# Kernel tuning notes

Hardware: AMD Instinct MI355X
Metric: run time of the kernel (lower is better)

Reference implementation:

```python
import jax, jax.numpy as jnp
import numpy as np

K = 16        # max_points
S = 3         # num_scales
D_MODEL = 256
KDIM = 16
TAU = 1e-4
B_BATCH = 512


def _boundaries(k):
    edges = [(i, j) for i in range(k) for j in range(i + 1, k)]
    tris = [(i, j, kk) for i in range(k) for j in range(i + 1, k) for kk in range(j + 1, k)]
    E, T = len(edges), len(tris)
    B1 = np.zeros((k, E), np.float32)
    for e, (i, j) in enumerate(edges):
        B1[i, e] = -1.0
        B1[j, e] = 1.0
    e2i = {e: idx for idx, e in enumerate(edges)}
    B2 = np.zeros((E, T), np.float32)
    for t, (i, j, kk) in enumerate(tris):
        B2[e2i[(j, kk)], t] = 1.0
        B2[e2i[(i, kk)], t] = -1.0
        B2[e2i[(i, j)], t] = 1.0
    e_i = np.array([e[0] for e in edges], np.int32)
    e_j = np.array([e[1] for e in edges], np.int32)
    t_ij = np.array([e2i[(a, b)] for (a, b, c) in tris], np.int32)
    t_jk = np.array([e2i[(b, c)] for (a, b, c) in tris], np.int32)
    t_ik = np.array([e2i[(a, c)] for (a, b, c) in tris], np.int32)
    return B1, B2, e_i, e_j, t_ij, t_jk, t_ik


def setup_inputs() -> dict:
    key = jax.random.key(0)
    ks = jax.random.split(key, 8)
    d = D_MODEL
    B1, B2, e_i, e_j, t_ij, t_jk, t_ik = _boundaries(K)

    def lin(kk, fin, fout):
        return jax.random.normal(kk, (fin, fout), jnp.float32) / np.sqrt(fin).astype(np.float32)

    return dict(
        x=jax.random.normal(ks[0], (B_BATCH, K, d), jnp.float32),
        mask=jnp.ones((B_BATCH, K), jnp.float32),
        B1=jnp.asarray(B1), B2=jnp.asarray(B2), abs_B1=jnp.asarray(np.abs(B1)),
        e_i=jnp.asarray(e_i), e_j=jnp.asarray(e_j),
        t_ij=jnp.asarray(t_ij), t_jk=jnp.asarray(t_jk), t_ik=jnp.asarray(t_ik),
        log_scales=jnp.linspace(-1.5, 1.5, S).astype(jnp.float32),
        Wg=lin(ks[1], d, KDIM), bg=jnp.zeros((KDIM,), jnp.float32),
        Wv0=lin(ks[2], d, d * S), bv0=jnp.zeros((d * S,), jnp.float32),
        We=lin(ks[3], d, d * S), be=jnp.zeros((d * S,), jnp.float32),
        Wout=lin(ks[4], 2 * S * d, d), bout=jnp.zeros((d,), jnp.float32),
        g1=jnp.ones((d,), jnp.float32), b1=jnp.zeros((d,), jnp.float32),
        g2=jnp.ones((d,), jnp.float32), b2=jnp.zeros((d,), jnp.float32),
        Wf1=lin(ks[5], d, 4 * d), bf1=jnp.zeros((4 * d,), jnp.float32),
        Wf2=lin(ks[6], 4 * d, d), bf2=jnp.zeros((d,), jnp.float32),
    )


def _layernorm(x, g, b):
    mu = jnp.mean(x, -1, keepdims=True)
    var = jnp.mean(jnp.square(x - mu), -1, keepdims=True)
    return (x - mu) * jax.lax.rsqrt(var + 1e-5) * g + b


def _forward(x, mask, B1, B2, abs_B1, e_i, e_j, t_ij, t_jk, t_ik,
             log_scales, Wg, bg, Wv0, bv0, We, be, Wout, bout,
             g1, b1, g2, b2, Wf1, bf1, Wf2, bf2):
    B, Kp, d = x.shape
    E = B1.shape[1]
    residual = x
    x_norm = _layernorm(x, g1, b1)
    P = x_norm @ Wg + bg                                   # (B,K,k_dim)
    mask2 = mask[:, :, None] * mask[:, None, :]            # (B,K,K)
    # cdist (safe sqrt: zero diag, no NaN grads)
    pn = jnp.sum(P * P, -1)
    d2 = jnp.maximum(pn[:, :, None] + pn[:, None, :] - 2.0 * jnp.einsum('bik,bjk->bij', P, P), 0.0)
    Dm = jnp.where(d2 > 0, jnp.sqrt(jnp.where(d2 > 0, d2, 1.0)), 0.0) * mask2
    sigma_sq = jnp.square(jnp.exp(log_scales))             # (S,)
    A = jnp.exp(-(Dm * Dm)[:, None] / (2.0 * sigma_sq[None, :, None, None] + 1e-8)) * mask2[:, None]  # (B,S,K,K)
    W1 = A[:, :, e_i, e_j]                                 # (B,S,E) edge gather
    W2 = W1[:, :, t_ij] * W1[:, :, t_jk] * W1[:, :, t_ik]  # (B,S,T) triangle weights
    V0 = (x_norm @ Wv0 + bv0).reshape(B, Kp, S, d).transpose(0, 2, 1, 3)         # (B,S,K,d)
    E_raw = jnp.einsum('ke,bkd->bed', abs_B1, x_norm)                            # (B,E,d)
    E_in = (E_raw @ We + be).reshape(B, E, S, d).transpose(0, 2, 1, 3)           # (B,S,E,d)
    # L0 = B1 diag(W1) B1^T + tau I
    L0 = jnp.einsum('ke,bse,me->bskm', B1, W1, B1) + TAU * jnp.eye(Kp, dtype=x.dtype)
    M0 = jnp.einsum('bskm,bsmd->bskd', L0, V0)
    # L1 = B1^T diag(mask) B1 + B2 diag(W2) B2^T + tau I
    term_down = jnp.einsum('ke,bk,kf->bef', B1, mask, B1)                        # (B,E,E)
    term_up = jnp.einsum('et,bst,ft->bsef', B2, W2, B2)                          # (B,S,E,E)
    L1 = term_down[:, None] + term_up + TAU * jnp.eye(E, dtype=x.dtype)
    M1 = jnp.einsum('bsef,bsfd->bsed', L1, E_in)
    M1n = jnp.einsum('ke,bsed->bskd', abs_B1, M1)                                # edges -> nodes
    node_cat = M0.transpose(0, 2, 1, 3).reshape(B, Kp, S * d)
    edge_cat = M1n.transpose(0, 2, 1, 3).reshape(B, Kp, S * d)
    attn = jnp.concatenate([node_cat, edge_cat], -1) @ Wout + bout
    x2 = residual + attn                                   # dropout is identity in eval
    h = jax.nn.gelu(_layernorm(x2, g2, b2) @ Wf1 + bf1, approximate=False) @ Wf2 + bf2
    return x2 + h


def reference(x, mask, B1, B2, abs_B1, e_i, e_j, t_ij, t_jk, t_ik,
              log_scales, Wg, bg, Wv0, bv0, We, be, Wout, bout,
              g1, b1, g2, b2, Wf1, bf1, Wf2, bf2):
    return _forward(x, mask, B1, B2, abs_B1, e_i, e_j, t_ij, t_jk, t_ik,
                    log_scales, Wg, bg, Wv0, bv0, We, be, Wout, bout,
                    g1, b1, g2, b2, Wf1, bf1, Wf2, bf2)
```

## Files before the change

### kernel.cpp

```cpp
#include <hip/hip_runtime.h>
#include <math.h>

#define KN 16
#define DM 256
#define NS 3
#define NE 120
#define NT_TRI 560
#define NBATCH 512
#define TAUF 1e-4f
#define KAUG 1600

typedef unsigned short ushort_t;
typedef __attribute__((ext_vector_type(8))) short short8v;
typedef __attribute__((ext_vector_type(4))) short short4v;
typedef __attribute__((ext_vector_type(4))) float f32x4;

#define OFF_WSTACK 0u
#define OFF_WF1T   819200u
#define OFF_WF2T   1343488u
#define OFF_TOPO   1867776u
#define OFF_Z      1875968u
#define OFF_H      1875968u
#define OFF_LN2    28090368u

__device__ __forceinline__ ushort_t f2bf(float f) {
    union { float f; unsigned int u; } v; v.f = f;
    unsigned int r = v.u + 0x7FFFu + ((v.u >> 16) & 1u);
    return (ushort_t)(r >> 16);
}
__device__ __forceinline__ void gload_lds16(const void* g, void* l) {
    auto gp = (const __attribute__((address_space(1))) unsigned int*)(unsigned long long)(g);
    auto lp = (__attribute__((address_space(3))) unsigned int*)(unsigned long long)(l);
    __builtin_amdgcn_global_load_lds(gp, lp, 16, 0, 0);
}

__global__ __launch_bounds__(256) void prep_kernel(
    const float* __restrict__ Wv0, const float* __restrict__ bv0,
    const float* __restrict__ We,  const float* __restrict__ be,
    const float* __restrict__ Wout,
    const float* __restrict__ Wf1, const float* __restrict__ Wf2,
    const int* __restrict__ e_i, const int* __restrict__ e_j,
    const int* __restrict__ t_ij, const int* __restrict__ t_jk, const int* __restrict__ t_ik,
    ushort_t* __restrict__ wstack, ushort_t* __restrict__ wf1t,
    ushort_t* __restrict__ wf2t,
    float* __restrict__ topoF, int* __restrict__ triPk)
{
    __shared__ float lhs[16][DM];
    __shared__ float tile[64][65];
    __shared__ int   eidxL[256];
    const int bid = blockIdx.x;
    const int j = threadIdx.x;

    if (bid == 230) {
        eidxL[j] = -1;
        __syncthreads();
        if (j < NE) {
            const int i = e_i[j], jn = e_j[j];
            eidxL[i*16 + jn] = j; eidxL[jn*16 + i] = j;
        }
        __syncthreads();
        const int n = j >> 4, m = j & 15;
        float q, p2, adj;
        if (n != m) {
            const int e = eidxL[j];
            if (e >= 0) { q = (m == e_j[e]) ? 1.f : -1.f; p2 = 1.f; adj = 1.f; }
            else        { q = 0.f; p2 = 0.f; adj = 0.f; }
        } else {
            q = 0.f; p2 = 0.f; adj = 0.f;
            for (int kk = 0; kk < KN; ++kk) {
                if (kk == n) continue;
                const int e = eidxL[n*16 + kk];
                if (e >= 0) { q += (n == e_j[e]) ? 1.f : -1.f; p2 += 1.f; }
            }
        }
        topoF[j] = q; topoF[256 + j] = p2; topoF[512 + j] = adj;
        for (int tt = j; tt < NT_TRI; tt += 256) {
            const int eij = t_ij[tt], ejk = t_jk[tt], eik = t_ik[tt];
            const int a0 = e_i[eij], a1 = e_j[eij];
            const int b0 = e_i[ejk], b1v = e_j[ejk];
            const int c0 = e_i[eik], c1 = e_j[eik];
            const int mid = (b0 == a0 || b0 == a1) ? b0 : b1v;
            triPk[2*tt]   = a0 | (a1 << 8) | (b0 << 16) | (b1v << 24);
            triPk[2*tt+1] = c0 | (c1 << 8) | (mid << 16);
        }
        return;
    }

    if (bid < 102) {
        const int m = bid / 17, by = bid % 17;
        const int path = m / 3, s = m % 3;
        const float* __restrict__ Wo = Wout + (size_t)m*DM*DM;
        if (by == 16) {
            const float* bv = (path == 0) ? bv0 : be;
            const float f = (path == 0) ? 1.0f : 0.5f;
            float acc = 0.f;
            for (int k = 0; k < DM; ++k)
                acc += bv[s*DM + k] * f * Wo[k*DM + j];
            wstack[(size_t)j*KAUG + 1536 + m] = f2bf(acc);
            if (m == 0)
                for (int c = 1542; c < KAUG; ++c)
                    wstack[(size_t)j*KAUG + c] = 0;
            return;
        }
        const float* src = (path == 0) ? Wv0 : We;
        const int i0 = by * 16;
        for (int r = 0; r < 16; ++r)
            lhs[r][j] = src[(size_t)(i0 + r)*(NS*DM) + s*DM + j];
        __syncthreads();
        float acc[16];
#pragma unroll
        for (int r = 0; r < 16; ++r) acc[r] = 0.f;
        for (int k = 0; k < DM; ++k) {
            const float w = Wo[k*DM + j];
#pragma unroll
            for (int r = 0; r < 16; ++r) acc[r] += lhs[r][k] * w;
        }
#pragma unroll
        for (int r = 0; r < 16; ++r)
            wstack[(size_t)j*KAUG + m*DM + i0 + r] = f2bf(acc[r]);
        return;
    }

    const float* in; ushort_t* outp; int R, C, rt, ct;
    if (bid < 166) {
        const int q = bid - 102;
        in = Wf1; outp = wf1t; R = 256; C = 1024;
        rt = (q >> 4) * 64; ct = (q & 15) * 64;
    } else {
        const int q = bid - 166;
        in = Wf2; outp = wf2t; R = 1024; C = 256;
        rt = (q >> 2) * 64; ct = (q & 3) * 64;
    }
#pragma unroll
    for (int q2 = 0; q2 < 16; ++q2) {
        const int idx = q2*256 + j;
        const int r = idx >> 6, c = idx & 63;
        tile[r][c] = in[(size_t)(rt + r)*C + ct + c];
    }
    __syncthreads();
#pragma unroll
    for (int q2 = 0; q2 < 16; ++q2) {
        const int idx = q2*256 + j;
        const int cc = idx >> 6, rr = idx & 63;
        outp[(size_t)(ct + cc)*R + rt + rr] = f2bf(tile[rr][cc]);
    }
}

__global__ __launch_bounds__(256) void attn_topo_kernel(
    const float* __restrict__ x, const float* __restrict__ mask,
    const float* __restrict__ log_scales,
    const float* __restrict__ Wg, const float* __restrict__ bg,
    const float* __restrict__ g1, const float* __restrict__ b1,
    const float* __restrict__ topoF, const int* __restrict__ triPk,
    ushort_t* __restrict__ Z)
{
    const int b = blockIdx.x;
    const int t = threadIdx.x;
    const int n = t >> 4, m = t & 15;

    __shared__ ushort_t xnbT[DM][16];
    __shared__ float Plds[KN][KN];
    __shared__ float mskL[KN];
    __shared__ float QL[256];
    __shared__ float P2L[256];
    __shared__ float adjL[256];
    __shared__ float sA[NS][KN][KN];
    __shared__ float Hupd[NS*KN];
    __shared__ ushort_t Tbf[6][KN][32];

    QL[t]  = topoF[t];
    P2L[t] = topoF[256 + t];
    adjL[t] = topoF[512 + t];
    if (t < KN) mskL[t] = mask[b*KN + t];

    float xv[16];
    {
        const int cg = m * 16;
        const float* xr = x + (size_t)(b*KN + n)*DM + cg;
        const f32x4 v0 = *(const f32x4*)(xr);
        const f32x4 v1 = *(const f32x4*)(xr + 4);
        const f32x4 v2 = *(const f32x4*)(xr + 8);
        const f32x4 v3 = *(const f32x4*)(xr + 12);
#pragma unroll
        for (int q = 0; q < 4; ++q) { xv[q] = v0[q]; xv[4+q] = v1[q]; xv[8+q] = v2[q]; xv[12+q] = v3[q]; }
        float ssum = 0.f;
#pragma unroll
        for (int q = 0; q < 16; ++q) ssum += xv[q];
#pragma unroll
        for (int o = 1; o < 16; o <<= 1) ssum += __shfl_xor(ssum, o);
        const float mu = ssum * (1.f/DM);
        float vsum = 0.f;
#pragma unroll
        for (int q = 0; q < 16; ++q) { const float d = xv[q]-mu; vsum += d*d; }
#pragma unroll
        for (int o = 1; o < 16; o <<= 1) vsum += __shfl_xor(vsum, o);
        const float rstd = rsqrtf(vsum*(1.f/DM) + 1e-5f);
        const f32x4 ga = *(const f32x4*)(g1 + cg),   gb = *(const f32x4*)(g1 + cg + 4);
        const f32x4 gc = *(const f32x4*)(g1 + cg + 8), gd = *(const f32x4*)(g1 + cg + 12);
        const f32x4 ba = *(const f32x4*)(b1 + cg),   bb = *(const f32x4*)(b1 + cg + 4);
        const f32x4 bc = *(const f32x4*)(b1 + cg + 8), bd = *(const f32x4*)(b1 + cg + 12);
        float gg[16], bbv[16];
#pragma unroll
        for (int q = 0; q < 4; ++q) {
            gg[q] = ga[q]; gg[4+q] = gb[q]; gg[8+q] = gc[q]; gg[12+q] = gd[q];
            bbv[q] = ba[q]; bbv[4+q] = bb[q]; bbv[8+q] = bc[q]; bbv[12+q] = bd[q];
        }
#pragma unroll
        for (int q = 0; q < 16; ++q) {
            xv[q] = (xv[q]-mu)*rstd*gg[q] + bbv[q];
            xnbT[cg + q][n] = f2bf(xv[q]);
        }
    }

    {
        float part[16];
#pragma unroll
        for (int c = 0; c < 16; ++c) part[c] = 0.f;
        const int cg = m * 16;
#pragma unroll
        for (int q = 0; q < 16; ++q) {
            const float xq = xv[q];
            const float* wr = Wg + (size_t)(cg + q)*KN;
            const f32x4 w0 = *(const f32x4*)(wr);
            const f32x4 w1 = *(const f32x4*)(wr + 4);
            const f32x4 w2 = *(const f32x4*)(wr + 8);
            const f32x4 w3 = *(const f32x4*)(wr + 12);
            part[0]  += xq*w0[0]; part[1]  += xq*w0[1]; part[2]  += xq*w0[2]; part[3]  += xq*w0[3];
            part[4]  += xq*w1[0]; part[5]  += xq*w1[1]; part[6]  += xq*w1[2]; part[7]  += xq*w1[3];
            part[8]  += xq*w2[0]; part[9]  += xq*w2[1]; part[10] += xq*w2[2]; part[11] += xq*w2[3];
            part[12] += xq*w3[0]; part[13] += xq*w3[1]; part[14] += xq*w3[2]; part[15] += xq*w3[3];
        }
        const int b0 = t & 1, b1b = (t>>1)&1, b2 = (t>>2)&1, b3 = (t>>3)&1;
        float p8[8];
#pragma unroll
        for (int c2 = 0; c2 < 8; ++c2) {
            const float keep = b0 ? part[2*c2+1] : part[2*c2];
            const float send = b0 ? part[2*c2]   : part[2*c2+1];
            p8[c2] = keep + __shfl_xor(send, 1);
        }
        float p4[4];
#pragma unroll
        for (int c2 = 0; c2 < 4; ++c2) {
            const float keep = b1b ? p8[2*c2+1] : p8[2*c2];
            const float send = b1b ? p8[2*c2]   : p8[2*c2+1];
            p4[c2] = keep + __shfl_xor(send, 2);
        }
        float p2v[2];
#pragma unroll
        for (int c2 = 0; c2 < 2; ++c2) {
            const float keep = b2 ? p4[2*c2+1] : p4[2*c2];
            const float send = b2 ? p4[2*c2]   : p4[2*c2+1];
            p2v[c2] = keep + __shfl_xor(send, 4);
        }
        const float keep = b3 ? p2v[1] : p2v[0];
        const float send = b3 ? p2v[0] : p2v[1];
        Plds[n][m] = keep + __shfl_xor(send, 8) + bg[m];
    }
    __syncthreads();

    float T0[NS], hq;
    {
        float d2 = 0.f;
#pragma unroll
        for (int k = 0; k < KN; ++k) {
            const float dd = Plds[n][k] - Plds[m][k];
            d2 += dd*dd;
        }
        const float m2v = mskL[n]*mskL[m];
        const float dm = (d2 > 0.f) ? sqrtf(d2)*m2v : 0.f;
        const float dmsq = dm*dm;
        const float adjv = adjL[t];
#pragma unroll
        for (int s = 0; s < NS; ++s) {
            const float sig2 = expf(2.f*log_scales[s]);
            const float a = expf(-dmsq/(2.f*sig2 + 1e-8f)) * m2v;
            sA[s][n][m] = a;
            const float am = a * adjv;
            float rsum = am;
#pragma unroll
            for (int o = 1; o < 16; o <<= 1) rsum += __shfl_xor(rsum, o);
            const float tv = (m == n) ? (TAUF + rsum) : (-am);
            T0[s] = tv;
            Tbf[s][n][m] = f2bf(tv);
        }
        hq = 0.f;
#pragma unroll
        for (int k = 0; k < KN; ++k)
            hq += mskL[k]*QL[n*16 + k]*QL[m*16 + k];
        if (t < NS*KN) Hupd[t] = 0.f;
#pragma unroll
        for (int idx = 0; idx < 6; ++idx) {
            const int e2 = idx*256 + t;
            Tbf[e2 >> 8][(e2 >> 4) & 15][16 + (e2 & 15)] = 0;
        }
    }
    __syncthreads();

    for (int tt = t; tt < NT_TRI; tt += 256) {
        const int w0 = triPk[2*tt], w1 = triPk[2*tt+1];
        const int a0 = w0 & 255, a1 = (w0 >> 8) & 255;
        const int b0 = (w0 >> 16) & 255, b1v = (w0 >> 24) & 255;
        const int c0 = w1 & 255, c1 = (w1 >> 8) & 255, mid = (w1 >> 16) & 255;
#pragma unroll
        for (int s = 0; s < NS; ++s)
            atomicAdd(&Hupd[s*KN + mid],
                      4.f * sA[s][a0][a1] * sA[s][b0][b1v] * sA[s][c0][c1]);
    }
    __syncthreads();

    ushort_t* Zb = Z + (size_t)b*KN*KAUG;
    {
        float T1[NS];
        const float p2v = P2L[t];
#pragma unroll
        for (int s = 0; s < NS; ++s) {
            const float tv = hq + TAUF*p2v + ((m == n) ? Hupd[s*KN + n] : 0.f);
            T1[s] = tv;
            Tbf[NS + s][n][m] = f2bf(tv);
        }
        float sv[6] = {T0[0], T0[1], T0[2], T1[0], T1[1], T1[2]};
#pragma unroll
        for (int q = 0; q < 6; ++q) {
            float v = sv[q];
#pragma unroll
            for (int o = 1; o < 16; o <<= 1) v += __shfl_xor(v, o);
            sv[q] = v;
        }
        const float wv = (m==0)?sv[0]:(m==1)?sv[1]:(m==2)?sv[2]:(m==3)?sv[3]:(m==4)?sv[4]:sv[5];
        if (m < 6) Zb[(size_t)n*KAUG + 1536 + m] = f2bf(wv);
        for (int idx = t; idx < 58*KN; idx += 256) {
            const int nn = idx / 58, c = 1542 + idx % 58;
            Zb[(size_t)nn*KAUG + c] = 0;
        }
    }
    __syncthreads();

    {
        const int w = t >> 6, l = t & 63;
        const int lr = l & 15, lk = l >> 4;
        short8v bfr[4];
#pragma unroll
        for (int q4 = 0; q4 < 4; ++q4) {
            const int jc = w*64 + q4*16 + lr;
            bfr[q4] = *(const short8v*)&xnbT[jc][(lk & 1)*8];
        }
#pragma unroll
        for (int m6 = 0; m6 < 6; ++m6) {
            const short8v af = *(const short8v*)&Tbf[m6][lr][lk*8];
#pragma unroll
            for (int q4 = 0; q4 < 4; ++q4) {
                f32x4 acc = {0.f,0.f,0.f,0.f};
                acc = __builtin_amdgcn_mfma_f32_16x16x32_bf16(af, bfr[q4], acc, 0, 0, 0);
                const int jc = w*64 + q4*16 + lr;
#pragma unroll
                for (int rg = 0; rg < 4; ++rg)
                    Zb[(size_t)(lk*4 + rg)*KAUG + m6*256 + jc] = f2bf(acc[rg]);
            }
        }
    }
}

template<int BM, int BN, int KD, int EPI>
__global__ __launch_bounds__(256) void gemm_lds(
    const ushort_t* __restrict__ A, const ushort_t* __restrict__ Bt,
    const float* __restrict__ bias, const float* __restrict__ resid,
    float* __restrict__ outF, ushort_t* __restrict__ outH, int ldo)
{
    constexpr int BK = 64;
    constexpr int MF = BM / 32, NF = BN / 32;
    __shared__ ushort_t lA[BM*BK];
    __shared__ ushort_t lB[BN*BK];
    const int t = threadIdx.x;
    const int w = t >> 6, l = t & 63;
    const int wm = w & 1, wn = w >> 1;
    const int lr = l & 15, lk = l >> 4;
    const int brow = blockIdx.x * BM;
    const int bcol = blockIdx.y * BN;

    f32x4 acc[MF][NF];
#pragma unroll
    for (int mf = 0; mf < MF; ++mf)
#pragma unroll
        for (int nt = 0; nt < NF; ++nt)
            acc[mf][nt] = (f32x4){0.f,0.f,0.f,0.f};

    const int byteoff = t * 16;

    for (int kc = 0; kc < KD/BK; ++kc) {
        if (kc) __syncthreads();
#pragma unroll
        for (int c = 0; c < BM/32; ++c) {
            const int bo = c*4096 + byteoff;
            const int row = bo >> 7, kb = bo & 127;
            gload_lds16(A + (size_t)(brow + row)*KD + kc*BK + (kb >> 1), lA + (bo >> 1));
        }
#pragma unroll
        for (int c = 0; c < BN/32; ++c) {
            const int bo = c*4096 + byteoff;
            const int row = bo >> 7, kb = bo & 127;
            gload_lds16(Bt + (size_t)(bcol + row)*KD + kc*BK + (kb >> 1), lB + (bo >> 1));
        }
        __syncthreads();
#pragma unroll
        for (int ks = 0; ks < 2; ++ks) {
            short8v af[MF], bfr[NF];
#pragma unroll
            for (int mf = 0; mf < MF; ++mf)
                af[mf] = *(const short8v*)(lA + (wm*(BM/2) + mf*16 + lr)*BK + ks*32 + lk*8);
#pragma unroll
            for (int nt = 0; nt < NF; ++nt)
                bfr[nt] = *(const short8v*)(lB + (wn*(BN/2) + nt*16 + lr)*BK + ks*32 + lk*8);
#pragma unroll
            for (int mf = 0; mf < MF; ++mf)
#pragma unroll
                for (int nt = 0; nt < NF; ++nt)
                    acc[mf][nt] = __builtin_amdgcn_mfma_f32_16x16x32_bf16(
                        af[mf], bfr[nt], acc[mf][nt], 0, 0, 0);
        }
    }

#pragma unroll
    for (int mf = 0; mf < MF; ++mf) {
#pragma unroll
        for (int nt = 0; nt < NF; ++nt) {
            const int col = bcol + wn*(BN/2) + nt*16 + lr;
#pragma unroll
            for (int rg = 0; rg < 4; ++rg) {
                const int row = brow + wm*(BM/2) + mf*16 + lk*4 + rg;
                const size_t o = (size_t)row * ldo + col;
                const float v = acc[mf][nt][rg];
                if (EPI == 1) {
                    const float u = v + bias[col];
                    const float a = 0.79788456080286536f*(u + 0.044715f*u*u*u);
                    outH[o] = f2bf(u / (1.f + __expf(-2.f*a)));
                } else if (EPI == 2) {
                    outF[o] = outF[o] + v + bias[col];
                } else {
                    outF[o] = resid[o] + v + bias[col];
                }
            }
        }
    }
}

__global__ __launch_bounds__(256) void ln_rows_kernel(
    const float* __restrict__ in, const float* __restrict__ g,
    const float* __restrict__ bvec, ushort_t* __restrict__ outv)
{
    const int row = blockIdx.x*4 + (threadIdx.x >> 6);
    const int l = threadIdx.x & 63;
    const float4 v = *(const float4*)(in + (size_t)row*DM + l*4);
    float s = v.x + v.y + v.z + v.w;
#pragma unroll
    for (int o = 1; o < 64; o <<= 1) s += __shfl_xor(s, o);
    const float mu = s * (1.f/DM);
    float d0 = v.x-mu, d1 = v.y-mu, d2 = v.z-mu, d3 = v.w-mu;
    float vs = d0*d0 + d1*d1 + d2*d2 + d3*d3;
#pragma unroll
    for (int o = 1; o < 64; o <<= 1) vs += __shfl_xor(vs, o);
    const float rstd = rsqrtf(vs*(1.f/DM) + 1e-5f);
    short4v o4;
    o4[0] = (short)f2bf(d0*rstd*g[l*4+0] + bvec[l*4+0]);
    o4[1] = (short)f2bf(d1*rstd*g[l*4+1] + bvec[l*4+1]);
    o4[2] = (short)f2bf(d2*rstd*g[l*4+2] + bvec[l*4+2]);
    o4[3] = (short)f2bf(d3*rstd*g[l*4+3] + bvec[l*4+3]);
    *(short4v*)(outv + (size_t)row*DM + l*4) = o4;
}

extern "C" void kernel_launch(void* const* d_in, const int* in_sizes, int n_in,
                              void* d_out, int out_size, void* d_ws, size_t ws_size,
                              hipStream_t stream) {
    const float* x          = (const float*)d_in[0];
    const float* mask       = (const float*)d_in[1];
    const int*   e_i        = (const int*)  d_in[5];
    const int*   e_j        = (const int*)  d_in[6];
    const int*   t_ij       = (const int*)  d_in[7];
    const int*   t_jk       = (const int*)  d_in[8];
    const int*   t_ik       = (const int*)  d_in[9];
    const float* log_scales = (const float*)d_in[10];
    const float* Wg         = (const float*)d_in[11];
    const float* bg         = (const float*)d_in[12];
    const float* Wv0        = (const float*)d_in[13];
    const float* bv0        = (const float*)d_in[14];
    const float* We         = (const float*)d_in[15];
    const float* be         = (const float*)d_in[16];
    const float* Wout       = (const float*)d_in[17];
    const float* bout       = (const float*)d_in[18];
    const float* g1         = (const float*)d_in[19];
    const float* b1         = (const float*)d_in[20];
    const float* g2         = (const float*)d_in[21];
    const float* b2         = (const float*)d_in[22];
    const float* Wf1        = (const float*)d_in[23];
    const float* bf1        = (const float*)d_in[24];
    const float* Wf2        = (const float*)d_in[25];
    const float* bf2        = (const float*)d_in[26];

    char* wsb = (char*)d_ws;
    ushort_t* wstack = (ushort_t*)(wsb + OFF_WSTACK);
    ushort_t* wf1t   = (ushort_t*)(wsb + OFF_WF1T);
    ushort_t* wf2t   = (ushort_t*)(wsb + OFF_WF2T);
    float*    topoF  = (float*)   (wsb + OFF_TOPO);
    int*      triPk  = (int*)     (wsb + OFF_TOPO + 3072);
    ushort_t* Z      = (ushort_t*)(wsb + OFF_Z);
    ushort_t* H      = (ushort_t*)(wsb + OFF_H);
    ushort_t* ln2    = (ushort_t*)(wsb + OFF_LN2);
    float*    out    = (float*)d_out;

    hipLaunchKernelGGL(prep_kernel, dim3(231), dim3(256), 0, stream,
                       Wv0, bv0, We, be, Wout, Wf1, Wf2,
                       e_i, e_j, t_ij, t_jk, t_ik,
                       wstack, wf1t, wf2t, topoF, triPk);
    hipLaunchKernelGGL(attn_topo_kernel, dim3(NBATCH), dim3(256), 0, stream,
                       x, mask, log_scales, Wg, bg, g1, b1, topoF, triPk, Z);
    hipLaunchKernelGGL((gemm_lds<64,64,KAUG,3>), dim3(128,4), dim3(256), 0, stream,
                       Z, wstack, bout, x, out, (ushort_t*)nullptr, 256);
    hipLaunchKernelGGL(ln_rows_kernel, dim3(2048), dim3(256), 0, stream,
                       out, g2, b2, ln2);
    hipLaunchKernelGGL((gemm_lds<128,128,256,1>), dim3(64,8), dim3(256), 0, stream,
                       ln2, wf1t, bf1, (const float*)nullptr,
                       (float*)nullptr, H, 1024);
    hipLaunchKernelGGL((gemm_lds<64,64,1024,2>), dim3(128,4), dim3(256), 0, stream,
                       H, wf2t, bf2, (const float*)nullptr,
                       out, (ushort_t*)nullptr, 256);
}
```

Before: 122.2 us.

## Fuse LayerNorm into FFN1 GEMM, swizzle LDS tiles, widen K-chunk, vectorize Z stores

The standalone LayerNorm kernel is folded into a new FFN1 GEMM that normalizes its 64-row A tile into LDS before the MMA loop. This removes one launch and the bf16 round trip of the normalized activations through global memory. The generic GEMM gains a BK template parameter, set to 128 for the two remaining instances, plus an XOR swizzle on LDS tiles to avoid bank conflicts. The attention kernel swaps its MFMA operands so Z is written as packed short4 vectors, padding the K dimension to 1664 (and xnbT to 32 columns) with zeros. The costs are more K-padding work in the first GEMM and more LDS per block, which may lower occupancy.

```diff
diff --git a/kernel.cpp b/kernel.cpp
--- a/kernel.cpp
+++ b/kernel.cpp
@@ -8,7 +8,7 @@
 #define NT_TRI 560
 #define NBATCH 512
 #define TAUF 1e-4f
-#define KAUG 1600
+#define KAUG 1664
 
 typedef unsigned short ushort_t;
 typedef __attribute__((ext_vector_type(8))) short short8v;
@@ -16,12 +16,11 @@
 typedef __attribute__((ext_vector_type(4))) float f32x4;
 
 #define OFF_WSTACK 0u
-#define OFF_WF1T   819200u
-#define OFF_WF2T   1343488u
-#define OFF_TOPO   1867776u
-#define OFF_Z      1875968u
-#define OFF_H      1875968u
-#define OFF_LN2    28090368u
+#define OFF_WF1T   851968u
+#define OFF_WF2T   1376256u
+#define OFF_TOPO   1900544u
+#define OFF_Z      1908736u
+#define OFF_H      1908736u
 
 __device__ __forceinline__ ushort_t f2bf(float f) {
     union { float f; unsigned int u; } v; v.f = f;
@@ -158,7 +157,7 @@
     const int t = threadIdx.x;
     const int n = t >> 4, m = t & 15;
 
-    __shared__ ushort_t xnbT[DM][16];
+    __shared__ ushort_t xnbT[DM][32];
     __shared__ float Plds[KN][KN];
     __shared__ float mskL[KN];
     __shared__ float QL[256];
@@ -172,6 +171,11 @@
     P2L[t] = topoF[256 + t];
     adjL[t] = topoF[512 + t];
     if (t < KN) mskL[t] = mask[b*KN + t];
+    {
+        const short8v z8 = {0,0,0,0,0,0,0,0};
+        *(short8v*)&xnbT[t][16] = z8;
+        *(short8v*)&xnbT[t][24] = z8;
+    }
 
     float xv[16];
     {
@@ -328,8 +332,8 @@
         }
         const float wv = (m==0)?sv[0]:(m==1)?sv[1]:(m==2)?sv[2]:(m==3)?sv[3]:(m==4)?sv[4]:sv[5];
         if (m < 6) Zb[(size_t)n*KAUG + 1536 + m] = f2bf(wv);
-        for (int idx = t; idx < 58*KN; idx += 256) {
-            const int nn = idx / 58, c = 1542 + idx % 58;
+        for (int idx = t; idx < 122*KN; idx += 256) {
+            const int nn = idx / 122, c = 1542 + idx % 122;
             Zb[(size_t)nn*KAUG + c] = 0;
         }
     }
@@ -338,36 +342,38 @@
     {
         const int w = t >> 6, l = t & 63;
         const int lr = l & 15, lk = l >> 4;
-        short8v bfr[4];
+        short8v bfrT[6];
+#pragma unroll
+        for (int m6 = 0; m6 < 6; ++m6)
+            bfrT[m6] = *(const short8v*)&Tbf[m6][lr][lk*8];
 #pragma unroll
         for (int q4 = 0; q4 < 4; ++q4) {
-            const int jc = w*64 + q4*16 + lr;
-            bfr[q4] = *(const short8v*)&xnbT[jc][(lk & 1)*8];
-        }
-#pragma unroll
-        for (int m6 = 0; m6 < 6; ++m6) {
-            const short8v af = *(const short8v*)&Tbf[m6][lr][lk*8];
-#pragma unroll
-            for (int q4 = 0; q4 < 4; ++q4) {
+            const int jb = w*64 + q4*16;
+            const short8v axn = *(const short8v*)&xnbT[jb + lr][lk*8];
+#pragma unroll
+            for (int m6 = 0; m6 < 6; ++m6) {
                 f32x4 acc = {0.f,0.f,0.f,0.f};
-                acc = __builtin_amdgcn_mfma_f32_16x16x32_bf16(af, bfr[q4], acc, 0, 0, 0);
-                const int jc = w*64 + q4*16 + lr;
-#pragma unroll
-                for (int rg = 0; rg < 4; ++rg)
-                    Zb[(size_t)(lk*4 + rg)*KAUG + m6*256 + jc] = f2bf(acc[rg]);
+                acc = __builtin_amdgcn_mfma_f32_16x16x32_bf16(axn, bfrT[m6], acc, 0, 0, 0);
+                short4v zv;
+#pragma unroll
+                for (int rg = 0; rg < 4; ++rg) zv[rg] = (short)f2bf(acc[rg]);
+                *(short4v*)(Zb + (size_t)lr*KAUG + m6*256 + jb + lk*4) = zv;
             }
         }
     }
 }
 
-template<int BM, int BN, int KD, int EPI>
+template<int BM, int BN, int BK, int KD, int EPI>
 __global__ __launch_bounds__(256) void gemm_lds(
     const ushort_t* __restrict__ A, const ushort_t* __restrict__ Bt,
     const float* __restrict__ bias, const float* __restrict__ resid,
     float* __restrict__ outF, ushort_t* __restrict__ outH, int ldo)
 {
-    constexpr int BK = 64;
-    constexpr int MF = BM / 32, NF = BN / 32;
+    constexpr int ROWB = BK*2;
+    constexpr int KS = BK/32;
+    constexpr int MF = BM/32, NF = BN/32;
+    constexpr int APASS = BM*ROWB/4096;
+    constexpr int BPASS = BN*ROWB/4096;
     __shared__ ushort_t lA[BM*BK];
     __shared__ ushort_t lB[BN*BK];
     const int t = threadIdx.x;
@@ -389,27 +395,35 @@
     for (int kc = 0; kc < KD/BK; ++kc) {
         if (kc) __syncthreads();
 #pragma unroll
-        for (int c = 0; c < BM/32; ++c) {
+        for (int c = 0; c < APASS; ++c) {
             const int bo = c*4096 + byteoff;
-            const int row = bo >> 7, kb = bo & 127;
-            gload_lds16(A + (size_t)(brow + row)*KD + kc*BK + (kb >> 1), lA + (bo >> 1));
-        }
-#pragma unroll
-        for (int c = 0; c < BN/32; ++c) {
+            const int row = bo / ROWB;
+            const int gs = ((bo % ROWB) >> 4) ^ (row & 7);
+            gload_lds16(A + (size_t)(brow + row)*KD + kc*BK + gs*8, lA + (bo >> 1));
+        }
+#pragma unroll
+        for (int c = 0; c < BPASS; ++c) {
             const int bo = c*4096 + byteoff;
-            const int row = bo >> 7, kb = bo & 127;
-            gload_lds16(Bt + (size_t)(bcol + row)*KD + kc*BK + (kb >> 1), lB + (bo >> 1));
+            const int row = bo / ROWB;
+            const int gs = ((bo % ROWB) >> 4) ^ (row & 7);
+            gload_lds16(Bt + (size_t)(bcol + row)*KD + kc*BK + gs*8, lB + (bo >> 1));
         }
         __syncthreads();
 #pragma unroll
-        for (int ks = 0; ks < 2; ++ks) {
+        for (int ks = 0; ks < KS; ++ks) {
             short8v af[MF], bfr[NF];
 #pragma unroll
-            for (int mf = 0; mf < MF; ++mf)
-                af[mf] = *(const short8v*)(lA + (wm*(BM/2) + mf*16 + lr)*BK + ks*32 + lk*8);
-#pragma unroll
-            for (int nt = 0; nt < NF; ++nt)
-                bfr[nt] = *(const short8v*)(lB + (wn*(BN/2) + nt*16 + lr)*BK + ks*32 + lk*8);
+            for (int mf = 0; mf < MF; ++mf) {
+                const int ra = wm*(BM/2) + mf*16 + lr;
+                const int gs = (ks*4 + lk) ^ (ra & 7);
+                af[mf] = *(const short8v*)(lA + ra*BK + gs*8);
+            }
+#pragma unroll
+            for (int nt = 0; nt < NF; ++nt) {
+                const int rb = wn*(BN/2) + nt*16 + lr;
+                const int gs = (ks*4 + lk) ^ (rb & 7);
+                bfr[nt] = *(const short8v*)(lB + rb*BK + gs*8);
+            }
 #pragma unroll
             for (int mf = 0; mf < MF; ++mf)
 #pragma unroll
@@ -429,11 +443,7 @@
                 const int row = brow + wm*(BM/2) + mf*16 + lk*4 + rg;
                 const size_t o = (size_t)row * ldo + col;
                 const float v = acc[mf][nt][rg];
-                if (EPI == 1) {
-                    const float u = v + bias[col];
-                    const float a = 0.79788456080286536f*(u + 0.044715f*u*u*u);
-                    outH[o] = f2bf(u / (1.f + __expf(-2.f*a)));
-                } else if (EPI == 2) {
+                if (EPI == 2) {
                     outF[o] = outF[o] + v + bias[col];
                 } else {
                     outF[o] = resid[o] + v + bias[col];
@@ -443,28 +453,118 @@
     }
 }
 
-__global__ __launch_bounds__(256) void ln_rows_kernel(
-    const float* __restrict__ in, const float* __restrict__ g,
-    const float* __restrict__ bvec, ushort_t* __restrict__ outv)
+__global__ __launch_bounds__(256) void gemm_ffn1(
+    const float* __restrict__ x2, const float* __restrict__ gv,
+    const float* __restrict__ bv,
+    const ushort_t* __restrict__ Bt, const float* __restrict__ bias,
+    ushort_t* __restrict__ outH)
 {
-    const int row = blockIdx.x*4 + (threadIdx.x >> 6);
-    const int l = threadIdx.x & 63;
-    const float4 v = *(const float4*)(in + (size_t)row*DM + l*4);
-    float s = v.x + v.y + v.z + v.w;
-#pragma unroll
-    for (int o = 1; o < 64; o <<= 1) s += __shfl_xor(s, o);
-    const float mu = s * (1.f/DM);
-    float d0 = v.x-mu, d1 = v.y-mu, d2 = v.z-mu, d3 = v.w-mu;
-    float vs = d0*d0 + d1*d1 + d2*d2 + d3*d3;
-#pragma unroll
-    for (int o = 1; o < 64; o <<= 1) vs += __shfl_xor(vs, o);
-    const float rstd = rsqrtf(vs*(1.f/DM) + 1e-5f);
-    short4v o4;
-    o4[0] = (short)f2bf(d0*rstd*g[l*4+0] + bvec[l*4+0]);
-    o4[1] = (short)f2bf(d1*rstd*g[l*4+1] + bvec[l*4+1]);
-    o4[2] = (short)f2bf(d2*rstd*g[l*4+2] + bvec[l*4+2]);
-    o4[3] = (short)f2bf(d3*rstd*g[l*4+3] + bvec[l*4+3]);
-    *(short4v*)(outv + (size_t)row*DM + l*4) = o4;
+    constexpr int BM = 64, BN = 128, KD = 256, BK = 64, ROWB = BK*2;
+    __shared__ ushort_t lnA[BM*KD];
+    __shared__ ushort_t lB[BN*BK];
+    const int t = threadIdx.x;
+    const int w = t >> 6, l = t & 63;
+    const int wm = w & 1, wn = w >> 1;
+    const int lr = l & 15, lk = l >> 4;
+    const int brow = blockIdx.x * BM;
+    const int bcol = blockIdx.y * BN;
+
+    {
+        const int row = t >> 2, c0 = (t & 3) * 64;
+        const float* xr = x2 + (size_t)(brow + row)*DM + c0;
+        f32x4 va[16];
+        float s = 0.f;
+#pragma unroll
+        for (int q = 0; q < 16; ++q) {
+            va[q] = *(const f32x4*)(xr + q*4);
+            s += va[q][0] + va[q][1] + va[q][2] + va[q][3];
+        }
+        s += __shfl_xor(s, 1); s += __shfl_xor(s, 2);
+        const float mu = s * (1.f/DM);
+        float vs = 0.f;
+#pragma unroll
+        for (int q = 0; q < 16; ++q) {
+#pragma unroll
+            for (int i = 0; i < 4; ++i) { const float d = va[q][i]-mu; vs += d*d; }
+        }
+        vs += __shfl_xor(vs, 1); vs += __shfl_xor(vs, 2);
+        const float rstd = rsqrtf(vs*(1.f/DM) + 1e-5f);
+#pragma unroll
+        for (int q = 0; q < 16; q += 2) {
+            short8v o;
+#pragma unroll
+            for (int i = 0; i < 4; ++i) {
+                const int c = c0 + q*4 + i;
+                o[i] = (short)f2bf((va[q][i]-mu)*rstd*gv[c] + bv[c]);
+            }
+#pragma unroll
+            for (int i = 0; i < 4; ++i) {
+                const int c = c0 + (q+1)*4 + i;
+                o[4+i] = (short)f2bf((va[q+1][i]-mu)*rstd*gv[c] + bv[c]);
+            }
+            const int g = (c0 >> 3) + (q >> 1);
+            const int gs = g ^ (row & 7);
+            *(short8v*)(lnA + row*KD + gs*8) = o;
+        }
+    }
+
+    f32x4 acc[2][4];
+#pragma unroll
+    for (int mf = 0; mf < 2; ++mf)
+#pragma unroll
+        for (int nt = 0; nt < 4; ++nt)
+            acc[mf][nt] = (f32x4){0.f,0.f,0.f,0.f};
+
+    const int byteoff = t * 16;
+    for (int kc = 0; kc < KD/BK; ++kc) {
+        __syncthreads();
+#pragma unroll
+        for (int c = 0; c < 4; ++c) {
+            const int bo = c*4096 + byteoff;
+            const int row = bo / ROWB;
+            const int gs = ((bo % ROWB) >> 4) ^ (row & 7);
+            gload_lds16(Bt + (size_t)(bcol + row)*KD + kc*BK + gs*8, lB + (bo >> 1));
+        }
+        __syncthreads();
+#pragma unroll
+        for (int ks = 0; ks < 2; ++ks) {
+            short8v af[2], bfr[4];
+#pragma unroll
+            for (int mf = 0; mf < 2; ++mf) {
+                const int ra = wm*32 + mf*16 + lr;
+                const int g = kc*8 + ks*4 + lk;
+                const int gs = g ^ (ra & 7);
+                af[mf] = *(const short8v*)(lnA + ra*KD + gs*8);
+            }
+#pragma unroll
+            for (int nt = 0; nt < 4; ++nt) {
+                const int rb = wn*64 + nt*16 + lr;
+                const int gs = (ks*4 + lk) ^ (rb & 7);
+                bfr[nt] = *(const short8v*)(lB + rb*BK + gs*8);
+            }
+#pragma unroll
+            for (int mf = 0; mf < 2; ++mf)
+#pragma unroll
+                for (int nt = 0; nt < 4; ++nt)
+                    acc[mf][nt] = __builtin_amdgcn_mfma_f32_16x16x32_bf16(
+                        af[mf], bfr[nt], acc[mf][nt], 0, 0, 0);
+        }
+    }
+
+#pragma unroll
+    for (int mf = 0; mf < 2; ++mf) {
+#pragma unroll
+        for (int nt = 0; nt < 4; ++nt) {
+            const int col = bcol + wn*64 + nt*16 + lr;
+#pragma unroll
+            for (int rg = 0; rg < 4; ++rg) {
+                const int row = brow + wm*32 + mf*16 + lk*4 + rg;
+                const float u = acc[mf][nt][rg] + bias[col];
+                const float a = 0.79788456080286536f*(u + 0.044715f*u*u*u);
+                outH[(size_t)row*1024 + col] = f2bf(u / (1.f + __expf(-2.f*a)));
+            }
+        }
+    }
 }
 
 extern "C" void kernel_launch(void* const* d_in, const int* in_sizes, int n_in,
@@ -503,7 +603,6 @@
     int*      triPk  = (int*)     (wsb + OFF_TOPO + 3072);
     ushort_t* Z      = (ushort_t*)(wsb + OFF_Z);
     ushort_t* H      = (ushort_t*)(wsb + OFF_H);
-    ushort_t* ln2    = (ushort_t*)(wsb + OFF_LN2);
     float*    out    = (float*)d_out;
 
     hipLaunchKernelGGL(prep_kernel, dim3(231), dim3(256), 0, stream,
@@ -512,14 +611,11 @@
                        wstack, wf1t, wf2t, topoF, triPk);
     hipLaunchKernelGGL(attn_topo_kernel, dim3(NBATCH), dim3(256), 0, stream,
                        x, mask, log_scales, Wg, bg, g1, b1, topoF, triPk, Z);
-    hipLaunchKernelGGL((gemm_lds<64,64,KAUG,3>), dim3(128,4), dim3(256), 0, stream,
+    hipLaunchKernelGGL((gemm_lds<64,64,128,KAUG,3>), dim3(128,4), dim3(256), 0, stream,
                        Z, wstack, bout, x, out, (ushort_t*)nullptr, 256);
-    hipLaunchKernelGGL(ln_rows_kernel, dim3(2048), dim3(256), 0, stream,
-                       out, g2, b2, ln2);
-    hipLaunchKernelGGL((gemm_lds<128,128,256,1>), dim3(64,8), dim3(256), 0, stream,
-                       ln2, wf1t, bf1, (const float*)nullptr,
-                       (float*)nullptr, H, 1024);
-    hipLaunchKernelGGL((gemm_lds<64,64,1024,2>), dim3(128,4), dim3(256), 0, stream,
+    hipLaunchKernelGGL(gemm_ffn1, dim3(128,8), dim3(256), 0, stream,
+                       out, g2, b2, wf1t, bf1, H);
+    hipLaunchKernelGGL((gemm_lds<64,64,128,1024,2>), dim3(128,4), dim3(256), 0, stream,
                        H, wf2t, bf2, (const float*)nullptr,
                        out, (ushort_t*)nullptr, 256);
 }
```

Result: no change. 123.5 us (+1.1%).

## Transpose MFMA operands for vectorized Z stores, add XCD swizzle, fast exp

Applied to the files above, without the earlier changes.

The attention-topology kernel's final MFMA swaps its operands so each lane holds four consecutive output columns. That allows one 8-byte vector store per tile instead of four strided 2-byte stores to Z. The x-normalized tile is padded to 32 with zeros to match the swapped operand layout. Separately, the GEMM remaps blockIdx.x with an XCD-aware swizzle to improve L2 locality, exp becomes __expf, and the prep kernel caches edge indices in LDS. The swizzle assumes gridDim.x is divisible by 8, and __expf slightly reduces accuracy.

```diff
diff --git a/kernel.cpp b/kernel.cpp
--- a/kernel.cpp
+++ b/kernel.cpp
@@ -32,6 +32,9 @@
     auto gp = (const __attribute__((address_space(1))) unsigned int*)(unsigned long long)(g);
     auto lp = (__attribute__((address_space(3))) unsigned int*)(unsigned long long)(l);
     __builtin_amdgcn_global_load_lds(gp, lp, 16, 0, 0);
+}
+__device__ __forceinline__ int xcd_swz(int b, int n) {
+    return (b & 7) * (n >> 3) + (b >> 3);
 }
 
 __global__ __launch_bounds__(256) void prep_kernel(
@@ -48,37 +51,39 @@
     __shared__ float lhs[16][DM];
     __shared__ float tile[64][65];
     __shared__ int   eidxL[256];
+    __shared__ int   eiL[NE], ejL[NE];
     const int bid = blockIdx.x;
     const int j = threadIdx.x;
 
     if (bid == 230) {
         eidxL[j] = -1;
+        if (j < NE) { eiL[j] = e_i[j]; ejL[j] = e_j[j]; }
         __syncthreads();
         if (j < NE) {
-            const int i = e_i[j], jn = e_j[j];
-            eidxL[i*16 + jn] = j; eidxL[jn*16 + i] = j;
+            eidxL[eiL[j]*16 + ejL[j]] = j;
+            eidxL[ejL[j]*16 + eiL[j]] = j;
         }
         __syncthreads();
         const int n = j >> 4, m = j & 15;
         float q, p2, adj;
         if (n != m) {
             const int e = eidxL[j];
-            if (e >= 0) { q = (m == e_j[e]) ? 1.f : -1.f; p2 = 1.f; adj = 1.f; }
+            if (e >= 0) { q = (m == ejL[e]) ? 1.f : -1.f; p2 = 1.f; adj = 1.f; }
             else        { q = 0.f; p2 = 0.f; adj = 0.f; }
         } else {
             q = 0.f; p2 = 0.f; adj = 0.f;
             for (int kk = 0; kk < KN; ++kk) {
                 if (kk == n) continue;
                 const int e = eidxL[n*16 + kk];
-                if (e >= 0) { q += (n == e_j[e]) ? 1.f : -1.f; p2 += 1.f; }
+                if (e >= 0) { q += (n == ejL[e]) ? 1.f : -1.f; p2 += 1.f; }
             }
         }
         topoF[j] = q; topoF[256 + j] = p2; topoF[512 + j] = adj;
         for (int tt = j; tt < NT_TRI; tt += 256) {
             const int eij = t_ij[tt], ejk = t_jk[tt], eik = t_ik[tt];
-            const int a0 = e_i[eij], a1 = e_j[eij];
-            const int b0 = e_i[ejk], b1v = e_j[ejk];
-            const int c0 = e_i[eik], c1 = e_j[eik];
+            const int a0 = eiL[eij], a1 = ejL[eij];
+            const int b0 = eiL[ejk], b1v = ejL[ejk];
+            const int c0 = eiL[eik], c1 = ejL[eik];
             const int mid = (b0 == a0 || b0 == a1) ? b0 : b1v;
             triPk[2*tt]   = a0 | (a1 << 8) | (b0 << 16) | (b1v << 24);
             triPk[2*tt+1] = c0 | (c1 << 8) | (mid << 16);
@@ -158,7 +163,7 @@
     const int t = threadIdx.x;
     const int n = t >> 4, m = t & 15;
 
-    __shared__ ushort_t xnbT[DM][16];
+    __shared__ ushort_t xnbT[DM][32];
     __shared__ float Plds[KN][KN];
     __shared__ float mskL[KN];
     __shared__ float QL[256];
@@ -172,6 +177,11 @@
     P2L[t] = topoF[256 + t];
     adjL[t] = topoF[512 + t];
     if (t < KN) mskL[t] = mask[b*KN + t];
+    {
+        const short8v z8 = {0,0,0,0,0,0,0,0};
+        *(short8v*)&xnbT[t][16] = z8;
+        *(short8v*)&xnbT[t][24] = z8;
+    }
 
     float xv[16];
     {
@@ -272,8 +282,8 @@
         const float adjv = adjL[t];
 #pragma unroll
         for (int s = 0; s < NS; ++s) {
-            const float sig2 = expf(2.f*log_scales[s]);
-            const float a = expf(-dmsq/(2.f*sig2 + 1e-8f)) * m2v;
+            const float sig2 = __expf(2.f*log_scales[s]);
+            const float a = __expf(-dmsq/(2.f*sig2 + 1e-8f)) * m2v;
             sA[s][n][m] = a;
             const float am = a * adjv;
             float rsum = am;
@@ -338,23 +348,22 @@
     {
         const int w = t >> 6, l = t & 63;
         const int lr = l & 15, lk = l >> 4;
-        short8v bfr[4];
+        short8v bfrT[6];
+#pragma unroll
+        for (int m6 = 0; m6 < 6; ++m6)
+            bfrT[m6] = *(const short8v*)&Tbf[m6][lr][lk*8];
 #pragma unroll
         for (int q4 = 0; q4 < 4; ++q4) {
-            const int jc = w*64 + q4*16 + lr;
-            bfr[q4] = *(const short8v*)&xnbT[jc][(lk & 1)*8];
-        }
-#pragma unroll
-        for (int m6 = 0; m6 < 6; ++m6) {
-            const short8v af = *(const short8v*)&Tbf[m6][lr][lk*8];
-#pragma unroll
-            for (int q4 = 0; q4 < 4; ++q4) {
+            const int jb = w*64 + q4*16;
+            const short8v axn = *(const short8v*)&xnbT[jb + lr][lk*8];
+#pragma unroll
+            for (int m6 = 0; m6 < 6; ++m6) {
                 f32x4 acc = {0.f,0.f,0.f,0.f};
-                acc = __builtin_amdgcn_mfma_f32_16x16x32_bf16(af, bfr[q4], acc, 0, 0, 0);
-                const int jc = w*64 + q4*16 + lr;
-#pragma unroll
-                for (int rg = 0; rg < 4; ++rg)
-                    Zb[(size_t)(lk*4 + rg)*KAUG + m6*256 + jc] = f2bf(acc[rg]);
+                acc = __builtin_amdgcn_mfma_f32_16x16x32_bf16(axn, bfrT[m6], acc, 0, 0, 0);
+                short4v zv;
+#pragma unroll
+                for (int rg = 0; rg < 4; ++rg) zv[rg] = (short)f2bf(acc[rg]);
+                *(short4v*)(Zb + (size_t)lr*KAUG + m6*256 + jb + lk*4) = zv;
             }
         }
     }
@@ -374,7 +383,8 @@
     const int w = t >> 6, l = t & 63;
     const int wm = w & 1, wn = w >> 1;
     const int lr = l & 15, lk = l >> 4;
-    const int brow = blockIdx.x * BM;
+    const int bxs = xcd_swz(blockIdx.x, gridDim.x);
+    const int brow = bxs * BM;
     const int bcol = blockIdx.y * BN;
 
     f32x4 acc[MF][NF];
```

Result: no change. 124.0 us (+1.5%).
